# Kernel optimization log

Measured on AMD Instinct MI355X. Metric: run time of the kernel, lower is better.

## Reference

```python
import jax, jax.numpy as jnp
import numpy as np
from jax import lax

B, S, H, W = 16, 5, 64, 64
D, DS, DEPTH, EXPAND, NC = 128, 16, 2, 2, 2


def _ln(x, w, b, eps=1e-5):
    m = x.mean(-1, keepdims=True)
    v = ((x - m) ** 2).mean(-1, keepdims=True)
    return (x - m) / jnp.sqrt(v + eps) * w + b


def _conv2d(x, w, b, stride, pad):
    y = lax.conv_general_dilated(x, w, (stride, stride), [(pad, pad), (pad, pad)],
                                 dimension_numbers=('NCHW', 'OIHW', 'NCHW'))
    return y + b[None, :, None, None]


def _convT2d(x, w, b):
    # torch ConvTranspose2d(k=4, s=2, p=1); w: (Cin, Cout, 4, 4)
    k = jnp.transpose(w[:, :, ::-1, ::-1], (1, 0, 2, 3))
    y = lax.conv_general_dilated(x, k, (1, 1), [(2, 2), (2, 2)], lhs_dilation=(2, 2),
                                 dimension_numbers=('NCHW', 'OIHW', 'NCHW'))
    return y + b[None, :, None, None]


def _dwconv1d(x, w, b):
    # x: [B, L, D]; torch depthwise Conv1d k=4 pad=3 then truncate to L == left-pad 3
    y = lax.conv_general_dilated(x.transpose(0, 2, 1), w, (1,), [(3, 0)],
                                 feature_group_count=w.shape[0],
                                 dimension_numbers=('NCH', 'OIH', 'NCH'))
    return (y + b[None, :, None]).transpose(0, 2, 1)


def _selective_scan(x, ln_w, ln_b, in_w, in_b, x_w, x_b, A_log, Dm, out_w, out_b):
    xn = _ln(x, ln_w, ln_b)
    xz = xn @ in_w.T + in_b
    xp, z = jnp.split(xz, 2, axis=-1)
    xp = jax.nn.silu(xp)
    z = jax.nn.sigmoid(z)
    u = xp @ x_w.T + x_b                        # [B, L, DS]
    a = jnp.exp(-jnp.exp(A_log))[0, 0]          # [DS] decay factor exp(A), A = -exp(A_log)

    def step(h, u_t):
        h = a * h + u_t
        return h, h

    _, hs = lax.scan(step, jnp.zeros((x.shape[0], DS), x.dtype), u.transpose(1, 0, 2))
    hs = hs.transpose(1, 0, 2)                  # [B, L, DS]
    y = (hs @ Dm) * z
    y = y @ out_w.T + out_b                     # dropout is identity at inference
    return x + y


def setup_inputs() -> dict:
    key = jax.random.key(0)
    ks = iter(jax.random.split(key, 64))

    def nrm(shape, scale=0.02):
        return (jax.random.normal(next(ks), shape) * scale).astype(jnp.float32)

    d, ds, hw = D, DS, H * W
    return {
        'x': jax.random.normal(next(ks), (B, S, H, W), dtype=jnp.float32),
        'emb_w': nrm((d, 1, 3, 3), 0.1), 'emb_b': jnp.zeros((d,), jnp.float32),
        'pos_embed': nrm((hw, d)), 'time_embed': nrm((S, d)),
        'blk_ln1_w': jnp.ones((DEPTH, d), jnp.float32), 'blk_ln1_b': jnp.zeros((DEPTH, d), jnp.float32),
        'blk_conv_w': nrm((DEPTH, d, 1, 4), 0.2), 'blk_conv_b': jnp.zeros((DEPTH, d), jnp.float32),
        'blk_sln_w': jnp.ones((DEPTH, d), jnp.float32), 'blk_sln_b': jnp.zeros((DEPTH, d), jnp.float32),
        'blk_A_log': nrm((DEPTH, 1, 1, ds), 0.5),
        'blk_D': nrm((DEPTH, ds, d), 0.1),
        'blk_in_w': nrm((DEPTH, 2 * d, d), 0.05), 'blk_in_b': jnp.zeros((DEPTH, 2 * d), jnp.float32),
        'blk_x_w': nrm((DEPTH, ds, d), 0.05), 'blk_x_b': jnp.zeros((DEPTH, ds), jnp.float32),
        'blk_out_w': nrm((DEPTH, d, d), 0.05), 'blk_out_b': jnp.zeros((DEPTH, d), jnp.float32),
        'blk_ln2_w': jnp.ones((DEPTH, d), jnp.float32), 'blk_ln2_b': jnp.zeros((DEPTH, d), jnp.float32),
        'blk_mlp_w1': nrm((DEPTH, EXPAND * d, d), 0.05), 'blk_mlp_b1': jnp.zeros((DEPTH, EXPAND * d), jnp.float32),
        'blk_mlp_w2': nrm((DEPTH, d, EXPAND * d), 0.05), 'blk_mlp_b2': jnp.zeros((DEPTH, d), jnp.float32),
        'down1_w': nrm((d, d, 3, 3), 0.05), 'down1_b': jnp.zeros((d,), jnp.float32),
        'down2_w': nrm((2 * d, d, 3, 3), 0.05), 'down2_b': jnp.zeros((2 * d,), jnp.float32),
        'bott_w': nrm((2 * d, 2 * d, 3, 3), 0.05), 'bott_b': jnp.zeros((2 * d,), jnp.float32),
        'up1_w': nrm((2 * d, d, 4, 4), 0.05), 'up1_b': jnp.zeros((d,), jnp.float32),
        'up2_w': nrm((2 * d, d, 4, 4), 0.05), 'up2_b': jnp.zeros((d,), jnp.float32),
        'final_w': nrm((NC, 2 * d, 1, 1), 0.05), 'final_b': jnp.zeros((NC,), jnp.float32),
    }


def reference(x, emb_w, emb_b, pos_embed, time_embed,
              blk_ln1_w, blk_ln1_b, blk_conv_w, blk_conv_b,
              blk_sln_w, blk_sln_b, blk_A_log, blk_D,
              blk_in_w, blk_in_b, blk_x_w, blk_x_b, blk_out_w, blk_out_b,
              blk_ln2_w, blk_ln2_b, blk_mlp_w1, blk_mlp_b1, blk_mlp_w2, blk_mlp_b2,
              down1_w, down1_b, down2_w, down2_b, bott_w, bott_b,
              up1_w, up1_b, up2_w, up2_b, final_w, final_b):
    b, s, h, w = x.shape
    # embed all frames at once (linear combination weights: 0.5 each, last frame 1.0)
    e = _conv2d(x.reshape(b * s, 1, h, w), emb_w, emb_b, 1, 1)      # [B*S, D, H, W]
    e = e.reshape(b, s, D, h * w).transpose(0, 1, 3, 2)              # [B, S, HW, D]
    e = e + pos_embed[None, None] + time_embed[:s][None, :, None, :]
    wts = jnp.where(jnp.arange(s) == s - 1, 1.0, 0.5).astype(x.dtype)
    emb = jnp.einsum('bsld,s->bld', e, wts)                          # [B, HW, D]
    for i in range(DEPTH):
        xn = _ln(emb, blk_ln1_w[i], blk_ln1_b[i])
        emb = emb + _dwconv1d(xn, blk_conv_w[i], blk_conv_b[i])
        emb = _selective_scan(emb, blk_sln_w[i], blk_sln_b[i], blk_in_w[i], blk_in_b[i],
                              blk_x_w[i], blk_x_b[i], blk_A_log[i], blk_D[i],
                              blk_out_w[i], blk_out_b[i])
        m = _ln(emb, blk_ln2_w[i], blk_ln2_b[i])
        m = jax.nn.gelu(m @ blk_mlp_w1[i].T + blk_mlp_b1[i], approximate=False)
        emb = emb + (m @ blk_mlp_w2[i].T + blk_mlp_b2[i])
    sp = emb.transpose(0, 2, 1).reshape(b, D, h, w)
    x1 = jax.nn.relu(_conv2d(sp, down1_w, down1_b, 2, 1))
    x2 = jax.nn.relu(_conv2d(x1, down2_w, down2_b, 2, 1))
    x2 = jax.nn.relu(_conv2d(x2, bott_w, bott_b, 1, 1))
    u1 = jax.nn.relu(_convT2d(x2, up1_w, up1_b))
    u1 = jnp.concatenate([u1, x1], axis=1)
    u2 = jax.nn.relu(_convT2d(u1, up2_w, up2_b))
    u2 = jnp.concatenate([u2, sp], axis=1)
    return _conv2d(u2, final_w, final_b, 1, 0)
```

## Files before the change

### kernel.cpp

```cpp
#include <hip/hip_runtime.h>
#include <cmath>

namespace {
constexpr int Bn = 16, Ln = 4096, Dn = 128, DSn = 16;
constexpr int Mtok = Bn * Ln;
}

typedef short bfx8 __attribute__((ext_vector_type(8)));
typedef float f32x4 __attribute__((ext_vector_type(4)));

static __device__ __forceinline__ ushort f2bf(float f) {
  union { float f; unsigned u; } v; v.f = f;
  unsigned r = v.u + 0x7fff + ((v.u >> 16) & 1);
  return (ushort)(r >> 16);
}
static __device__ __forceinline__ float bf2f(ushort u) {
  union { unsigned u; float f; } v; v.u = ((unsigned)u) << 16;
  return v.f;
}

__global__ void k_prep(const float* __restrict__ inw, const float* __restrict__ outw,
                       const float* __restrict__ m1, const float* __restrict__ m2,
                       const float* __restrict__ xw, const float* __restrict__ cw,
                       const float* __restrict__ d1, const float* __restrict__ d2,
                       const float* __restrict__ bo, const float* __restrict__ u1,
                       const float* __restrict__ u2, ushort* __restrict__ W3,
                       float* __restrict__ CWT) {
  int i = blockIdx.x * 256 + threadIdx.x;
  if (i < 65536) { W3[i] = f2bf(inw[i]); return; }
  if (i < 98304) { W3[i] = f2bf(outw[i - 65536]); return; }
  if (i < 163840) { W3[i] = f2bf(m1[i - 98304]); return; }
  if (i < 229376) { W3[i] = f2bf(m2[i - 163840]); return; }
  if (i < 233472) { W3[i] = f2bf(xw[i - 229376]); return; }
  if (i < 234496) {
    int j = i - 233472; int blk = j >> 9, r = j & 511, d = r >> 2, k = r & 3;
    CWT[blk * 512 + k * 128 + d] = cw[j]; return;
  }
  if (i < 381952) {
    int j = i - 234496; int co = j / (128 * 9); int r = j - co * (128 * 9);
    int ci = r / 9, tap = r - ci * 9;
    W3[233472 + ((size_t)tap * 128 + co) * 128 + ci] = f2bf(d1[j]); return;
  }
  if (i < 676864) {
    int j = i - 381952; int co = j / (128 * 9); int r = j - co * (128 * 9);
    int ci = r / 9, tap = r - ci * 9;
    W3[380928 + ((size_t)tap * 256 + co) * 128 + ci] = f2bf(d2[j]); return;
  }
  if (i < 1266688) {
    int j = i - 676864; int co = j / (256 * 9); int r = j - co * (256 * 9);
    int ci = r / 9, tap = r - ci * 9;
    W3[675840 + ((size_t)tap * 256 + co) * 256 + ci] = f2bf(bo[j]); return;
  }
  if (i < 1790976) {
    int j = i - 1266688; int ci = j / (128 * 16); int r = j - ci * (128 * 16);
    int co = r >> 4, tap = r & 15;
    W3[1265664 + ((size_t)tap * 128 + co) * 256 + ci] = f2bf(u1[j]); return;
  }
  if (i < 2315264) {
    int j = i - 1790976; int ci = j / (128 * 16); int r = j - ci * (128 * 16);
    int co = r >> 4, tap = r & 15;
    W3[1789952 + ((size_t)tap * 128 + co) * 256 + ci] = f2bf(u2[j]); return;
  }
}

__global__ void k_combine(const float* __restrict__ x, float* __restrict__ xc) {
  int i = blockIdx.x * 256 + threadIdx.x;
  int b = i >> 12, p = i & 4095;
  const float* xb = x + (size_t)b * 5 * Ln + p;
  xc[i] = 0.5f * (xb[0] + xb[Ln] + xb[2 * Ln] + xb[3 * Ln]) + xb[4 * Ln];
}

__global__ __launch_bounds__(256) void k_embedln(
    const float* __restrict__ xc, const float* __restrict__ ew, const float* __restrict__ eb,
    const float* __restrict__ pos, const float* __restrict__ te,
    const float* __restrict__ lw, const float* __restrict__ lb,
    float* __restrict__ emb, ushort* __restrict__ xn) {
  int tok = blockIdx.x * 8 + (threadIdx.x >> 5);
  int ln = threadIdx.x & 31;
  int b = tok >> 12, l = tok & 4095;
  int h = l >> 6, w = l & 63;
  const float* xb = xc + b * 4096;
  float v[9];
#pragma unroll
  for (int dy = 0; dy < 3; dy++)
#pragma unroll
    for (int dx = 0; dx < 3; dx++) {
      int y = h + dy - 1, xx = w + dx - 1;
      v[dy * 3 + dx] = (y >= 0 && y < 64 && xx >= 0 && xx < 64) ? xb[y * 64 + xx] : 0.f;
    }
  int d0 = ln * 4;
  float o[4]; float s = 0.f, sq = 0.f;
#pragma unroll
  for (int e = 0; e < 4; e++) {
    int d = d0 + e;
    float a = 0.f;
#pragma unroll
    for (int k = 0; k < 9; k++) a += v[k] * ew[d * 9 + k];
    float ts = 0.5f * (te[d] + te[128 + d] + te[256 + d] + te[384 + d]) + te[512 + d];
    float r = a + 3.f * eb[d] + 3.f * pos[l * 128 + d] + ts;
    o[e] = r; s += r; sq += r * r;
  }
  float4 f4; f4.x = o[0]; f4.y = o[1]; f4.z = o[2]; f4.w = o[3];
  *(float4*)(emb + (size_t)tok * 128 + d0) = f4;
#pragma unroll
  for (int off = 16; off; off >>= 1) { s += __shfl_xor(s, off); sq += __shfl_xor(sq, off); }
  float m = s * (1.f / 128.f);
  float var = sq * (1.f / 128.f) - m * m;
  float rs = rsqrtf(var + 1e-5f);
  ushort4 u;
  u.x = f2bf((o[0] - m) * rs * lw[d0 + 0] + lb[d0 + 0]);
  u.y = f2bf((o[1] - m) * rs * lw[d0 + 1] + lb[d0 + 1]);
  u.z = f2bf((o[2] - m) * rs * lw[d0 + 2] + lb[d0 + 2]);
  u.w = f2bf((o[3] - m) * rs * lw[d0 + 3] + lb[d0 + 3]);
  *(ushort4*)(xn + (size_t)tok * 128 + d0) = u;
}

__global__ __launch_bounds__(256) void k_fuse1(
    const ushort* __restrict__ xn1, float* __restrict__ emb, ushort* __restrict__ xn2,
    const float* __restrict__ cwT, const float* __restrict__ cb,
    const float* __restrict__ sw, const float* __restrict__ sb) {
  int i = blockIdx.x * 256 + threadIdx.x;
  int g = i & 15, tok = i >> 4, d0 = g * 8, l = tok & 4095;
  const ushort* p = xn1 + (size_t)tok * 128 + d0;
  const bfx8 zf = {0, 0, 0, 0, 0, 0, 0, 0};
  bfx8 v0 = *(const bfx8*)p;
  bfx8 v1 = (l >= 1) ? *(const bfx8*)(p - 128) : zf;
  bfx8 v2 = (l >= 2) ? *(const bfx8*)(p - 256) : zf;
  bfx8 v3 = (l >= 3) ? *(const bfx8*)(p - 384) : zf;
  float* ep = emb + (size_t)tok * 128 + d0;
  float4 e0 = *(const float4*)ep;
  float4 e1 = *(const float4*)(ep + 4);
  float ev[8] = {e0.x, e0.y, e0.z, e0.w, e1.x, e1.y, e1.z, e1.w};
  float nv[8]; float s = 0.f, sq = 0.f;
#pragma unroll
  for (int e = 0; e < 8; e++) {
    int d = d0 + e;
    float c = cb[d] + cwT[3 * 128 + d] * bf2f((ushort)v0[e]) + cwT[2 * 128 + d] * bf2f((ushort)v1[e]) +
              cwT[1 * 128 + d] * bf2f((ushort)v2[e]) + cwT[0 * 128 + d] * bf2f((ushort)v3[e]);
    nv[e] = ev[e] + c;
    s += nv[e]; sq += nv[e] * nv[e];
  }
  float4 w0; w0.x = nv[0]; w0.y = nv[1]; w0.z = nv[2]; w0.w = nv[3];
  float4 w1; w1.x = nv[4]; w1.y = nv[5]; w1.z = nv[6]; w1.w = nv[7];
  *(float4*)ep = w0;
  *(float4*)(ep + 4) = w1;
#pragma unroll
  for (int off = 8; off; off >>= 1) { s += __shfl_xor(s, off); sq += __shfl_xor(sq, off); }
  float m = s * (1.f / 128.f);
  float var = sq * (1.f / 128.f) - m * m;
  float rs = rsqrtf(var + 1e-5f);
  bfx8 r8;
#pragma unroll
  for (int e = 0; e < 8; e++) {
    int d = d0 + e;
    r8[e] = (short)f2bf((nv[e] - m) * rs * sw[d] + sb[d]);
  }
  *(bfx8*)(xn2 + (size_t)tok * 128 + d0) = r8;
}

template <int MODE, int K>
__global__ __launch_bounds__(256) void k_mgemm(const ushort* __restrict__ A, const ushort* __restrict__ W,
                                               const float* __restrict__ bias, void* __restrict__ outv,
                                               void* __restrict__ out2v, float* __restrict__ emb,
                                               const float* __restrict__ lw, const float* __restrict__ lb) {
  __shared__ float red[2][128][2];
  const int t = threadIdx.x;
  const int l = t & 63, wv = t >> 6;
  const int l15 = l & 15, q = l >> 4;
  const int wm = wv >> 1, wn = wv & 1;
  const int m0 = blockIdx.x * 128 + wm * 64;
  const int n0 = blockIdx.y * 128 + wn * 64;
  f32x4 acc[4][4] = {};
  const ushort* Ab = A + (size_t)(m0 + l15) * K + q * 8;
  const ushort* Wb = W + (size_t)(n0 + l15) * K + q * 8;
#pragma unroll
  for (int k0 = 0; k0 < K; k0 += 32) {
    bfx8 a[4], b[4];
#pragma unroll
    for (int mf = 0; mf < 4; mf++) a[mf] = *(const bfx8*)(Ab + (size_t)mf * 16 * K + k0);
#pragma unroll
    for (int nf = 0; nf < 4; nf++) b[nf] = *(const bfx8*)(Wb + (size_t)nf * 16 * K + k0);
#pragma unroll
    for (int mf = 0; mf < 4; mf++)
#pragma unroll
      for (int nf = 0; nf < 4; nf++)
        acc[mf][nf] = __builtin_amdgcn_mfma_f32_16x16x32_bf16(a[mf], b[nf], acc[mf][nf], 0, 0, 0);
  }
  if constexpr (MODE == 1 || MODE == 2) {
#pragma unroll
    for (int mf = 0; mf < 4; mf++) {
#pragma unroll
      for (int nf = 0; nf < 4; nf++) {
        const int col = n0 + nf * 16 + l15;
        const float bb = bias[col];
#pragma unroll
        for (int r = 0; r < 4; r++) {
          const int row = m0 + mf * 16 + q * 4 + r;
          float v = acc[mf][nf][r] + bb;
          if (MODE == 1) {
            if (col < 128) {
              ((ushort*)outv)[(size_t)row * 128 + col] = f2bf(v / (1.f + expf(-v)));
            } else {
              ((ushort*)out2v)[(size_t)row * 128 + col - 128] = f2bf(1.f / (1.f + expf(-v)));
            }
          } else {
            ((ushort*)outv)[(size_t)row * 256 + col] = f2bf(0.5f * v * (1.f + erff(v * 0.7071067811865475f)));
          }
        }
      }
    }
  } else {
    float sv[4][4], qv[4][4];
#pragma unroll
    for (int mf = 0; mf < 4; mf++)
#pragma unroll
      for (int r = 0; r < 4; r++) { sv[mf][r] = 0.f; qv[mf][r] = 0.f; }
#pragma unroll
    for (int mf = 0; mf < 4; mf++) {
#pragma unroll
      for (int nf = 0; nf < 4; nf++) {
        const int col = n0 + nf * 16 + l15;
        const float bb = bias[col];
#pragma unroll
        for (int r = 0; r < 4; r++) {
          const int row = m0 + mf * 16 + q * 4 + r;
          float v = acc[mf][nf][r] + bb + emb[(size_t)row * 128 + col];
          acc[mf][nf][r] = v;
          sv[mf][r] += v; qv[mf][r] += v * v;
        }
      }
    }
    if constexpr (MODE == 5) {
#pragma unroll
      for (int mf = 0; mf < 4; mf++)
#pragma unroll
        for (int r = 0; r < 4; r++) {
#pragma unroll
          for (int off = 1; off < 16; off <<= 1) {
            sv[mf][r] += __shfl_xor(sv[mf][r], off);
            qv[mf][r] += __shfl_xor(qv[mf][r], off);
          }
          if (l15 == 0) {
            int rowl = wm * 64 + mf * 16 + q * 4 + r;
            red[0][rowl][wn] = sv[mf][r];
            red[1][rowl][wn] = qv[mf][r];
          }
        }
      __syncthreads();
    }
#pragma unroll
    for (int mf = 0; mf < 4; mf++)
#pragma unroll
      for (int r = 0; r < 4; r++) {
        const int rowl = wm * 64 + mf * 16 + q * 4 + r;
        const int row = blockIdx.x * 128 + rowl;
        float mm = 0.f, rs = 0.f;
        if constexpr (MODE == 5) {
          float ts = red[0][rowl][0] + red[0][rowl][1];
          float tq = red[1][rowl][0] + red[1][rowl][1];
          mm = ts * (1.f / 128.f);
          float var = tq * (1.f / 128.f) - mm * mm;
          rs = rsqrtf(var + 1e-5f);
        }
#pragma unroll
        for (int nf = 0; nf < 4; nf++) {
          const int col = n0 + nf * 16 + l15;
          float v = acc[mf][nf][r];
          emb[(size_t)row * 128 + col] = v;
          if constexpr (MODE == 5)
            ((ushort*)out2v)[(size_t)row * 128 + col] = f2bf((v - mm) * rs * lw[col] + lb[col]);
          else
            ((ushort*)out2v)[(size_t)row * 256 + 128 + col] = f2bf(v);
        }
      }
  }
}

__global__ __launch_bounds__(256) void k_ub(const ushort* __restrict__ XP, const ushort* __restrict__ xw,
                                            const float* __restrict__ xb, float* __restrict__ UT) {
  __shared__ float xs[16 * 132];
  __shared__ float wsm[16 * 129];
  const int m0 = blockIdx.x * 16;
  const int t = threadIdx.x;
  for (int idx = t; idx < 2048; idx += 256) {
    wsm[(idx >> 7) * 129 + (idx & 127)] = bf2f(xw[idx]);
    xs[(idx >> 7) * 132 + (idx & 127)] = bf2f(XP[(size_t)m0 * 128 + idx]);
  }
  __syncthreads();
  const int ds = t & 15, ml = t >> 4;
  float acc = 0.f;
#pragma unroll 16
  for (int k = 0; k < 128; k++) acc += xs[ml * 132 + k] * wsm[ds * 129 + k];
  const int b = m0 >> 12, l0 = m0 & 4095;
  UT[((size_t)(b * 16 + ds)) * 4096 + l0 + ml] = acc + xb[ds];
}

__global__ __launch_bounds__(64) void k_scan(const float* __restrict__ UT, float* __restrict__ HST,
                                             const float* __restrict__ A_log) {
  const int b = blockIdx.x >> 4, ds = blockIdx.x & 15;
  const int tid = threadIdx.x;
  const float a = expf(-expf(A_log[ds]));
  const float4* ut4 = (const float4*)(UT + ((size_t)(b * 16 + ds)) * 4096 + tid * 64);
  float r[64];
#pragma unroll
  for (int j4 = 0; j4 < 16; j4++) {
    float4 v = ut4[j4];
    r[j4 * 4 + 0] = v.x; r[j4 * 4 + 1] = v.y; r[j4 * 4 + 2] = v.z; r[j4 * 4 + 3] = v.w;
  }
  float h = 0.f;
#pragma unroll
  for (int j = 0; j < 64; j++) { h = a * h + r[j]; r[j] = h; }
  float a64 = a;
#pragma unroll
  for (int qq = 0; qq < 6; qq++) a64 *= a64;
  float Ac = a64, Bc = h;
#pragma unroll
  for (int off = 1; off < 64; off <<= 1) {
    float Ap = __shfl_up(Ac, off);
    float Bp = __shfl_up(Bc, off);
    if (tid >= off) { Bc = Ac * Bp + Bc; Ac = Ac * Ap; }
  }
  float carry = __shfl_up(Bc, 1);
  if (tid == 0) carry = 0.f;
  float p = a;
#pragma unroll
  for (int j = 0; j < 64; j++) { r[j] += p * carry; p *= a; }
  float4* hb4 = (float4*)(HST + ((size_t)(b * 16 + ds)) * 4096 + tid * 64);
#pragma unroll
  for (int j4 = 0; j4 < 16; j4++) {
    float4 v; v.x = r[j4 * 4 + 0]; v.y = r[j4 * 4 + 1]; v.z = r[j4 * 4 + 2]; v.w = r[j4 * 4 + 3];
    hb4[j4] = v;
  }
}

__global__ __launch_bounds__(256) void k_yb(const float* __restrict__ HST, const float* __restrict__ Dm_,
                                            const ushort* __restrict__ Z, ushort* __restrict__ Y) {
  const int m = blockIdx.x * 2 + (threadIdx.x >> 7);
  const int d = threadIdx.x & 127;
  const int b = m >> 12, l = m & 4095;
  const float* hb = HST + (size_t)b * 16 * Ln + l;
  float acc = 0.f;
#pragma unroll
  for (int s = 0; s < 16; s++) acc += hb[(size_t)s * Ln] * Dm_[s * 128 + d];
  const size_t o = (size_t)m * 128 + d;
  Y[o] = f2bf(acc * bf2f(Z[o]));
}

template <int MODE, int OTH, int OTW, int CIN>
__global__ __launch_bounds__(256) void k_cv(
    const ushort* __restrict__ in, ushort* __restrict__ out,
    const ushort* __restrict__ wt, const float* __restrict__ bias,
    int Hi, int Wi, int CP, int CO, int CPo, int COo, int Cout,
    int nsp, int nspx, long ibs, long obs) {
  constexpr int ITH = (MODE == 1) ? (2 * OTH + 1) : (OTH + 2);
  constexpr int ITW = (MODE == 1) ? (2 * OTW + 1) : (OTW + 2);
  constexpr int NPIX = ITH * ITW;
  constexpr int SPF = OTH * OTW / 16;
  constexpr int NTAPS = (MODE == 2) ? 4 : 9;
  constexpr int NCH = CIN / 32;
  __shared__ __attribute__((aligned(16))) ushort lds[NPIX * 40];
  const int t = threadIdx.x;
  const int w = t >> 6, l = t & 63;
  const int l15 = l & 15, q = l >> 4;
  const int b = blockIdx.z;
  const int py = (MODE == 2) ? ((int)blockIdx.y >> 1) : 0;
  const int px = (MODE == 2) ? ((int)blockIdx.y & 1) : 0;
  const int cb = blockIdx.x / nsp;
  const int spt = blockIdx.x - cb * nsp;
  const int spy = spt / nspx, spx = spt - spy * nspx;
  const int n0 = cb * 64 + w * 16;
  const int y0 = spy * OTH, x0 = spx * OTW;
  const int gy0 = (MODE == 1) ? (2 * y0 - 1) : (y0 - 1);
  const int gx0 = (MODE == 1) ? (2 * x0 - 1) : (x0 - 1);
  const ushort* ib = in + (size_t)b * ibs;
  f32x4 acc[SPF] = {};
  int abase[SPF];
#pragma unroll
  for (int af = 0; af < SPF; af++) {
    int p = af * 16 + l15;
    int ty = p / OTW, tx = p % OTW;
    int sy = (MODE == 1) ? (2 * ty) : ty;
    int sx = (MODE == 1) ? (2 * tx) : tx;
    abase[af] = (sy * ITW + sx) * 40 + q * 8;
  }
  for (int c = 0; c < NCH; c++) {
    const int k0 = c * 32;
    __syncthreads();
    for (int idx = t; idx < NPIX * 4; idx += 256) {
      int pix = idx >> 2, qq = idx & 3;
      int sy = pix / ITW, sx = pix - sy * ITW;
      int gy = gy0 + sy, gx = gx0 + sx;
      bfx8 v = {0, 0, 0, 0, 0, 0, 0, 0};
      if ((unsigned)gy < (unsigned)Hi && (unsigned)gx < (unsigned)Wi)
        v = *(const bfx8*)(ib + (size_t)(gy * Wi + gx) * CP + CO + k0 + qq * 8);
      *(bfx8*)&lds[pix * 40 + qq * 8] = v;
    }
    __syncthreads();
#pragma unroll
    for (int tap = 0; tap < NTAPS; tap++) {
      const int dy = (MODE == 2) ? (tap >> 1) : (tap / 3);
      const int dx = (MODE == 2) ? (tap & 1) : (tap - (tap / 3) * 3);
      const int tapw = (MODE == 2) ? ((3 - py - 2 * dy) * 4 + (3 - px - 2 * dx)) : tap;
      const int toff = (MODE == 2) ? (((py + dy) * ITW + (px + dx)) * 40)
                                   : ((dy * ITW + dx) * 40);
      bfx8 bv = *(const bfx8*)(wt + ((size_t)tapw * Cout + n0 + l15) * CIN + k0 + q * 8);
#pragma unroll
      for (int af = 0; af < SPF; af++) {
        bfx8 av = *(const bfx8*)&lds[abase[af] + toff];
        acc[af] = __builtin_amdgcn_mfma_f32_16x16x32_bf16(av, bv, acc[af], 0, 0, 0);
      }
    }
  }
  const float bb = bias[n0 + l15];
  ushort* ob = out + (size_t)b * obs + COo + n0 + l15;
#pragma unroll
  for (int af = 0; af < SPF; af++) {
#pragma unroll
    for (int r = 0; r < 4; r++) {
      int p = af * 16 + q * 4 + r;
      int ty = p / OTW, tx = p % OTW;
      int oy, ox, Wo;
      if (MODE == 2) { oy = (y0 + ty) * 2 + py; ox = (x0 + tx) * 2 + px; Wo = Wi * 2; }
      else if (MODE == 1) { oy = y0 + ty; ox = x0 + tx; Wo = Wi / 2; }
      else { oy = y0 + ty; ox = x0 + tx; Wo = Wi; }
      ob[(size_t)(oy * Wo + ox) * CPo] = f2bf(fmaxf(acc[af][r] + bb, 0.f));
    }
  }
}

__global__ void k_final2(const ushort* __restrict__ in, const float* __restrict__ w,
                         const float* __restrict__ bias, float* __restrict__ out) {
  int i = blockIdx.x * 256 + threadIdx.x;
  int b = i >> 12, p = i & 4095;
  const ushort* row = in + (size_t)i * 256;
  float a0 = bias[0], a1 = bias[1];
  for (int c = 0; c < 256; c += 4) {
    ushort4 u = *(const ushort4*)(row + c);
    float4 w0 = *(const float4*)(w + c);
    float4 w1 = *(const float4*)(w + 256 + c);
    float f0 = bf2f(u.x), f1 = bf2f(u.y), f2 = bf2f(u.z), f3 = bf2f(u.w);
    a0 += f0 * w0.x + f1 * w0.y + f2 * w0.z + f3 * w0.w;
    a1 += f0 * w1.x + f1 * w1.y + f2 * w1.z + f3 * w1.w;
  }
  out[(size_t)b * 8192 + p] = a0;
  out[(size_t)b * 8192 + 4096 + p] = a1;
}

extern "C" void kernel_launch(void* const* d_in, const int* in_sizes, int n_in,
                              void* d_out, int out_size, void* d_ws, size_t ws_size,
                              hipStream_t stream) {
  (void)in_sizes; (void)n_in; (void)out_size; (void)ws_size;
  const float* x          = (const float*)d_in[0];
  const float* emb_w      = (const float*)d_in[1];
  const float* emb_b      = (const float*)d_in[2];
  const float* pos_embed  = (const float*)d_in[3];
  const float* time_embed = (const float*)d_in[4];
  const float* blk_ln1_w  = (const float*)d_in[5];
  const float* blk_ln1_b  = (const float*)d_in[6];
  const float* blk_conv_w = (const float*)d_in[7];
  const float* blk_conv_b = (const float*)d_in[8];
  const float* blk_sln_w  = (const float*)d_in[9];
  const float* blk_sln_b  = (const float*)d_in[10];
  const float* blk_A_log  = (const float*)d_in[11];
  const float* blk_D      = (const float*)d_in[12];
  const float* blk_in_w   = (const float*)d_in[13];
  const float* blk_in_b   = (const float*)d_in[14];
  const float* blk_x_w    = (const float*)d_in[15];
  const float* blk_x_b    = (const float*)d_in[16];
  const float* blk_out_w  = (const float*)d_in[17];
  const float* blk_out_b  = (const float*)d_in[18];
  const float* blk_ln2_w  = (const float*)d_in[19];
  const float* blk_ln2_b  = (const float*)d_in[20];
  const float* blk_mlp_w1 = (const float*)d_in[21];
  const float* blk_mlp_b1 = (const float*)d_in[22];
  const float* blk_mlp_w2 = (const float*)d_in[23];
  const float* blk_mlp_b2 = (const float*)d_in[24];
  const float* down1_w    = (const float*)d_in[25];
  const float* down1_b    = (const float*)d_in[26];
  const float* down2_w    = (const float*)d_in[27];
  const float* down2_b    = (const float*)d_in[28];
  const float* bott_w     = (const float*)d_in[29];
  const float* bott_b     = (const float*)d_in[30];
  const float* up1_w      = (const float*)d_in[31];
  const float* up1_b      = (const float*)d_in[32];
  const float* up2_w      = (const float*)d_in[33];
  const float* up2_b      = (const float*)d_in[34];
  const float* final_w    = (const float*)d_in[35];
  const float* final_b    = (const float*)d_in[36];

  float* ws = (float*)d_ws;
  constexpr size_t F = 1u << 20;
  float* EMB = ws;
  ushort* XN1 = (ushort*)(ws + 8 * F);
  ushort* XN2 = XN1 + 8 * F;
  ushort* XPu = (ushort*)(ws + 16 * F);
  ushort* Zu  = XPu + 8 * F;
  ushort* MH  = XPu;
  ushort* W3  = (ushort*)(ws + 24 * F);
  float* Ubuf = ws + 32 * F;
  float* HST  = ws + 33 * F;

  ushort* Wi  = W3;
  ushort* Wo  = W3 + 65536;
  ushort* Wm1 = W3 + 98304;
  ushort* Wm2 = W3 + 163840;
  ushort* Wx  = W3 + 229376;
  ushort* Wd1 = W3 + 233472;
  ushort* Wd2 = W3 + 380928;
  ushort* Wb9 = W3 + 675840;
  ushort* Wu1 = W3 + 1265664;
  ushort* Wu2 = W3 + 1789952;
  float*  CWT = (float*)(W3 + 2314240);

  k_prep<<<9044, 256, 0, stream>>>(blk_in_w, blk_out_w, blk_mlp_w1, blk_mlp_w2, blk_x_w,
                                   blk_conv_w, down1_w, down2_w, bott_w, up1_w, up2_w, W3, CWT);
  k_combine<<<256, 256, 0, stream>>>(x, Ubuf);
  k_embedln<<<8192, 256, 0, stream>>>(Ubuf, emb_w, emb_b, pos_embed, time_embed,
                                      blk_ln1_w, blk_ln1_b, EMB, XN1);

  ushort* U2C = XPu;
  for (int i = 0; i < 2; i++) {
    k_fuse1<<<4096, 256, 0, stream>>>(XN1, EMB, XN2, CWT + i * 512, blk_conv_b + i * Dn,
                                      blk_sln_w + i * Dn, blk_sln_b + i * Dn);
    k_mgemm<1, 128><<<dim3(512, 2), 256, 0, stream>>>(XN2, Wi + i * 32768, blk_in_b + i * 256,
                                                      XPu, Zu, nullptr, nullptr, nullptr);
    k_ub<<<4096, 256, 0, stream>>>(XPu, Wx + i * 2048, blk_x_b + i * DSn, Ubuf);
    k_scan<<<256, 64, 0, stream>>>(Ubuf, HST, blk_A_log + i * DSn);
    k_yb<<<32768, 256, 0, stream>>>(HST, blk_D + i * DSn * Dn, Zu, XN2);
    k_mgemm<5, 128><<<dim3(512, 1), 256, 0, stream>>>(XN2, Wo + i * 16384, blk_out_b + i * Dn,
                                                      nullptr, XN1, EMB,
                                                      blk_ln2_w + i * Dn, blk_ln2_b + i * Dn);
    k_mgemm<2, 128><<<dim3(512, 2), 256, 0, stream>>>(XN1, Wm1 + i * 32768, blk_mlp_b1 + i * 256,
                                                      MH, nullptr, nullptr, nullptr, nullptr);
    if (i == 0)
      k_mgemm<5, 256><<<dim3(512, 1), 256, 0, stream>>>(MH, Wm2 + i * 32768, blk_mlp_b2 + i * Dn,
                                                        nullptr, XN1, EMB,
                                                        blk_ln1_w + Dn, blk_ln1_b + Dn);
    else
      k_mgemm<4, 256><<<dim3(512, 1), 256, 0, stream>>>(MH, Wm2 + i * 32768, blk_mlp_b2 + i * Dn,
                                                        nullptr, U2C, EMB, nullptr, nullptr);
  }

  ushort* U1C = XN1;
  ushort* X2b = XN1 + 8388608;
  ushort* X3b = X2b + 1048576;

  k_cv<1, 8, 8, 128><<<dim3(2 * 16, 1, 16), 256, 0, stream>>>(
      U2C, U1C, Wd1, down1_b, 64, 64, 256, 128, 256, 128, 128,
      16, 4, 64L * 64 * 256, 32L * 32 * 256);
  k_cv<1, 8, 8, 128><<<dim3(4 * 4, 1, 16), 256, 0, stream>>>(
      U1C, X2b, Wd2, down2_b, 32, 32, 256, 128, 256, 0, 256,
      4, 2, 32L * 32 * 256, 16L * 16 * 256);
  k_cv<0, 8, 8, 256><<<dim3(4 * 4, 1, 16), 256, 0, stream>>>(
      X2b, X3b, Wb9, bott_b, 16, 16, 256, 0, 256, 0, 256,
      4, 2, 16L * 16 * 256, 16L * 16 * 256);
  k_cv<2, 8, 16, 256><<<dim3(2 * 2, 4, 16), 256, 0, stream>>>(
      X3b, U1C, Wu1, up1_b, 16, 16, 256, 0, 256, 0, 128,
      2, 1, 16L * 16 * 256, 32L * 32 * 256);
  k_cv<2, 16, 16, 256><<<dim3(2 * 4, 4, 16), 256, 0, stream>>>(
      U1C, U2C, Wu2, up2_b, 32, 32, 256, 0, 256, 0, 128,
      4, 2, 32L * 32 * 256, 64L * 64 * 256);

  k_final2<<<256, 256, 0, stream>>>(U2C, final_w, final_b, (float*)d_out);
}
```

Baseline: 554.5 us.

## Fuse in-proj with x-proj GEMM and out-proj with MLP-up GEMM via LDS

The input-projection GEMM now keeps the SiLU branch tile in shared memory and computes the 16-wide x-projection with MFMA in the same kernel. This removes the separate k_ub kernel and the XP round trip through global memory. The output projection plus LayerNorm is likewise fused with the first MLP GEMM plus GELU, keeping the normalized tile in LDS so XN1 is no longer written and reread. The conv kernels gain a waves-per-block template parameter, and the smaller decoder layers now launch more blocks of 128 threads. The cost is extra LDS and register pressure in the fused kernels, and a serial second GEMM per block.

```diff
diff --git a/kernel.cpp b/kernel.cpp
--- a/kernel.cpp
+++ b/kernel.cpp
@@ -4,6 +4,7 @@
 namespace {
 constexpr int Bn = 16, Ln = 4096, Dn = 128, DSn = 16;
 constexpr int Mtok = Bn * Ln;
+constexpr int SLS = 138;
 }
 
 typedef short bfx8 __attribute__((ext_vector_type(8)));
@@ -158,10 +159,206 @@
   *(bfx8*)(xn2 + (size_t)tok * 128 + d0) = r8;
 }
 
+__global__ __launch_bounds__(256) void k_gemm_xz(
+    const ushort* __restrict__ A, const ushort* __restrict__ W, const float* __restrict__ bias,
+    ushort* __restrict__ Zu, const ushort* __restrict__ xw, const float* __restrict__ xb,
+    float* __restrict__ UT) {
+  __shared__ ushort sl[128 * SLS];
+  const int t = threadIdx.x;
+  const int l = t & 63, wv = t >> 6;
+  const int l15 = l & 15, q = l >> 4;
+  const int wm = wv >> 1, wn = wv & 1;
+  const int m0 = blockIdx.x * 128 + wm * 64;
+  const int n0 = blockIdx.y * 128 + wn * 64;
+  f32x4 acc[4][4] = {};
+  const ushort* Ab = A + (size_t)(m0 + l15) * 128 + q * 8;
+  const ushort* Wb = W + (size_t)(n0 + l15) * 128 + q * 8;
+#pragma unroll
+  for (int k0 = 0; k0 < 128; k0 += 32) {
+    bfx8 a[4], b[4];
+#pragma unroll
+    for (int mf = 0; mf < 4; mf++) a[mf] = *(const bfx8*)(Ab + (size_t)mf * 16 * 128 + k0);
+#pragma unroll
+    for (int nf = 0; nf < 4; nf++) b[nf] = *(const bfx8*)(Wb + (size_t)nf * 16 * 128 + k0);
+#pragma unroll
+    for (int mf = 0; mf < 4; mf++)
+#pragma unroll
+      for (int nf = 0; nf < 4; nf++)
+        acc[mf][nf] = __builtin_amdgcn_mfma_f32_16x16x32_bf16(a[mf], b[nf], acc[mf][nf], 0, 0, 0);
+  }
+  if (blockIdx.y == 1) {
+#pragma unroll
+    for (int mf = 0; mf < 4; mf++)
+#pragma unroll
+      for (int nf = 0; nf < 4; nf++) {
+        const int col = n0 + nf * 16 + l15;
+        const float bb = bias[col];
+#pragma unroll
+        for (int r = 0; r < 4; r++) {
+          const int row = m0 + mf * 16 + q * 4 + r;
+          float v = acc[mf][nf][r] + bb;
+          Zu[(size_t)row * 128 + col - 128] = f2bf(1.f / (1.f + expf(-v)));
+        }
+      }
+    return;
+  }
+#pragma unroll
+  for (int mf = 0; mf < 4; mf++)
+#pragma unroll
+    for (int nf = 0; nf < 4; nf++) {
+      const int col = wn * 64 + nf * 16 + l15;
+      const float bb = bias[col];
+#pragma unroll
+      for (int r = 0; r < 4; r++) {
+        const int rowl = wm * 64 + mf * 16 + q * 4 + r;
+        float v = acc[mf][nf][r] + bb;
+        sl[rowl * SLS + col] = f2bf(v / (1.f + expf(-v)));
+      }
+    }
+  __syncthreads();
+  f32x4 pu[2] = {};
+#pragma unroll
+  for (int k0 = 0; k0 < 128; k0 += 32) {
+    bfx8 bx_ = *(const bfx8*)(xw + l15 * 128 + k0 + q * 8);
+#pragma unroll
+    for (int mi = 0; mi < 2; mi++) {
+      bfx8 a2 = *(const bfx8*)&sl[(wv * 32 + mi * 16 + l15) * SLS + k0 + q * 8];
+      pu[mi] = __builtin_amdgcn_mfma_f32_16x16x32_bf16(a2, bx_, pu[mi], 0, 0, 0);
+    }
+  }
+  const float ub = xb[l15];
+#pragma unroll
+  for (int mi = 0; mi < 2; mi++)
+#pragma unroll
+    for (int r = 0; r < 4; r++) {
+      int token = blockIdx.x * 128 + wv * 32 + mi * 16 + q * 4 + r;
+      int b = token >> 12, ll = token & 4095;
+      UT[((size_t)(b * 16 + l15)) * 4096 + ll] = pu[mi][r] + ub;
+    }
+}
+
+__global__ __launch_bounds__(256) void k_gemm_om(
+    const ushort* __restrict__ A, const ushort* __restrict__ W1, const float* __restrict__ b1,
+    float* __restrict__ emb, const float* __restrict__ lw, const float* __restrict__ lb,
+    const ushort* __restrict__ W2, const float* __restrict__ b2, ushort* __restrict__ MH) {
+  __shared__ ushort sl[128 * SLS];
+  __shared__ float red[2][128][2];
+  const int t = threadIdx.x;
+  const int l = t & 63, wv = t >> 6;
+  const int l15 = l & 15, q = l >> 4;
+  const int wm = wv >> 1, wn = wv & 1;
+  const int m0 = blockIdx.x * 128 + wm * 64;
+  const int n0 = wn * 64;
+  {
+    f32x4 acc[4][4] = {};
+    const ushort* Ab = A + (size_t)(m0 + l15) * 128 + q * 8;
+    const ushort* Wb = W1 + (size_t)(n0 + l15) * 128 + q * 8;
+#pragma unroll
+    for (int k0 = 0; k0 < 128; k0 += 32) {
+      bfx8 a[4], b[4];
+#pragma unroll
+      for (int mf = 0; mf < 4; mf++) a[mf] = *(const bfx8*)(Ab + (size_t)mf * 16 * 128 + k0);
+#pragma unroll
+      for (int nf = 0; nf < 4; nf++) b[nf] = *(const bfx8*)(Wb + (size_t)nf * 16 * 128 + k0);
+#pragma unroll
+      for (int mf = 0; mf < 4; mf++)
+#pragma unroll
+        for (int nf = 0; nf < 4; nf++)
+          acc[mf][nf] = __builtin_amdgcn_mfma_f32_16x16x32_bf16(a[mf], b[nf], acc[mf][nf], 0, 0, 0);
+    }
+    float sv[4][4], qv[4][4];
+#pragma unroll
+    for (int mf = 0; mf < 4; mf++)
+#pragma unroll
+      for (int r = 0; r < 4; r++) { sv[mf][r] = 0.f; qv[mf][r] = 0.f; }
+#pragma unroll
+    for (int mf = 0; mf < 4; mf++)
+#pragma unroll
+      for (int nf = 0; nf < 4; nf++) {
+        const int col = n0 + nf * 16 + l15;
+        const float bb = b1[col];
+#pragma unroll
+        for (int r = 0; r < 4; r++) {
+          const int row = m0 + mf * 16 + q * 4 + r;
+          float v = acc[mf][nf][r] + bb + emb[(size_t)row * 128 + col];
+          acc[mf][nf][r] = v;
+          sv[mf][r] += v; qv[mf][r] += v * v;
+        }
+      }
+#pragma unroll
+    for (int mf = 0; mf < 4; mf++)
+#pragma unroll
+      for (int r = 0; r < 4; r++) {
+#pragma unroll
+        for (int off = 1; off < 16; off <<= 1) {
+          sv[mf][r] += __shfl_xor(sv[mf][r], off);
+          qv[mf][r] += __shfl_xor(qv[mf][r], off);
+        }
+        if (l15 == 0) {
+          int rowl = wm * 64 + mf * 16 + q * 4 + r;
+          red[0][rowl][wn] = sv[mf][r];
+          red[1][rowl][wn] = qv[mf][r];
+        }
+      }
+    __syncthreads();
+#pragma unroll
+    for (int mf = 0; mf < 4; mf++)
+#pragma unroll
+      for (int r = 0; r < 4; r++) {
+        const int rowl = wm * 64 + mf * 16 + q * 4 + r;
+        const int row = blockIdx.x * 128 + rowl;
+        float ts = red[0][rowl][0] + red[0][rowl][1];
+        float tq = red[1][rowl][0] + red[1][rowl][1];
+        float mm = ts * (1.f / 128.f);
+        float var = tq * (1.f / 128.f) - mm * mm;
+        float rs = rsqrtf(var + 1e-5f);
+#pragma unroll
+        for (int nf = 0; nf < 4; nf++) {
+          const int col = n0 + nf * 16 + l15;
+          float v = acc[mf][nf][r];
+          emb[(size_t)row * 128 + col] = v;
+          sl[rowl * SLS + col] = f2bf((v - mm) * rs * lw[col] + lb[col]);
+        }
+      }
+  }
+  __syncthreads();
+#pragma unroll
+  for (int p = 0; p < 2; p++) {
+    f32x4 acc2[2][8] = {};
+#pragma unroll
+    for (int k0 = 0; k0 < 128; k0 += 32) {
+      bfx8 a2[2];
+#pragma unroll
+      for (int mi = 0; mi < 2; mi++)
+        a2[mi] = *(const bfx8*)&sl[(wv * 32 + mi * 16 + l15) * SLS + k0 + q * 8];
+#pragma unroll
+      for (int nf = 0; nf < 8; nf++) {
+        bfx8 b2v = *(const bfx8*)(W2 + (size_t)(p * 128 + nf * 16 + l15) * 128 + k0 + q * 8);
+#pragma unroll
+        for (int mi = 0; mi < 2; mi++)
+          acc2[mi][nf] = __builtin_amdgcn_mfma_f32_16x16x32_bf16(a2[mi], b2v, acc2[mi][nf], 0, 0, 0);
+      }
+    }
+#pragma unroll
+    for (int mi = 0; mi < 2; mi++)
+#pragma unroll
+      for (int nf = 0; nf < 8; nf++) {
+        const int col = p * 128 + nf * 16 + l15;
+        const float bb = b2[col];
+#pragma unroll
+        for (int r = 0; r < 4; r++) {
+          const int row = blockIdx.x * 128 + wv * 32 + mi * 16 + q * 4 + r;
+          float v = acc2[mi][nf][r] + bb;
+          MH[(size_t)row * 256 + col] = f2bf(0.5f * v * (1.f + erff(v * 0.7071067811865475f)));
+        }
+      }
+  }
+}
+
 template <int MODE, int K>
 __global__ __launch_bounds__(256) void k_mgemm(const ushort* __restrict__ A, const ushort* __restrict__ W,
-                                               const float* __restrict__ bias, void* __restrict__ outv,
-                                               void* __restrict__ out2v, float* __restrict__ emb,
+                                               const float* __restrict__ bias, void* __restrict__ out2v,
+                                               float* __restrict__ emb,
                                                const float* __restrict__ lw, const float* __restrict__ lb) {
   __shared__ float red[2][128][2];
   const int t = threadIdx.x;
@@ -169,7 +366,7 @@
   const int l15 = l & 15, q = l >> 4;
   const int wm = wv >> 1, wn = wv & 1;
   const int m0 = blockIdx.x * 128 + wm * 64;
-  const int n0 = blockIdx.y * 128 + wn * 64;
+  const int n0 = wn * 64;
   f32x4 acc[4][4] = {};
   const ushort* Ab = A + (size_t)(m0 + l15) * K + q * 8;
   const ushort* Wb = W + (size_t)(n0 + l15) * K + q * 8;
@@ -186,113 +383,68 @@
       for (int nf = 0; nf < 4; nf++)
         acc[mf][nf] = __builtin_amdgcn_mfma_f32_16x16x32_bf16(a[mf], b[nf], acc[mf][nf], 0, 0, 0);
   }
-  if constexpr (MODE == 1 || MODE == 2) {
-#pragma unroll
-    for (int mf = 0; mf < 4; mf++) {
+  float sv[4][4], qv[4][4];
+#pragma unroll
+  for (int mf = 0; mf < 4; mf++)
+#pragma unroll
+    for (int r = 0; r < 4; r++) { sv[mf][r] = 0.f; qv[mf][r] = 0.f; }
+#pragma unroll
+  for (int mf = 0; mf < 4; mf++)
+#pragma unroll
+    for (int nf = 0; nf < 4; nf++) {
+      const int col = n0 + nf * 16 + l15;
+      const float bb = bias[col];
+#pragma unroll
+      for (int r = 0; r < 4; r++) {
+        const int row = m0 + mf * 16 + q * 4 + r;
+        float v = acc[mf][nf][r] + bb + emb[(size_t)row * 128 + col];
+        acc[mf][nf][r] = v;
+        sv[mf][r] += v; qv[mf][r] += v * v;
+      }
+    }
+  if constexpr (MODE == 5) {
+#pragma unroll
+    for (int mf = 0; mf < 4; mf++)
+#pragma unroll
+      for (int r = 0; r < 4; r++) {
+#pragma unroll
+        for (int off = 1; off < 16; off <<= 1) {
+          sv[mf][r] += __shfl_xor(sv[mf][r], off);
+          qv[mf][r] += __shfl_xor(qv[mf][r], off);
+        }
+        if (l15 == 0) {
+          int rowl = wm * 64 + mf * 16 + q * 4 + r;
+          red[0][rowl][wn] = sv[mf][r];
+          red[1][rowl][wn] = qv[mf][r];
+        }
+      }
+    __syncthreads();
+  }
+#pragma unroll
+  for (int mf = 0; mf < 4; mf++)
+#pragma unroll
+    for (int r = 0; r < 4; r++) {
+      const int rowl = wm * 64 + mf * 16 + q * 4 + r;
+      const int row = blockIdx.x * 128 + rowl;
+      float mm = 0.f, rs = 0.f;
+      if constexpr (MODE == 5) {
+        float ts = red[0][rowl][0] + red[0][rowl][1];
+        float tq = red[1][rowl][0] + red[1][rowl][1];
+        mm = ts * (1.f / 128.f);
+        float var = tq * (1.f / 128.f) - mm * mm;
+        rs = rsqrtf(var + 1e-5f);
+      }
 #pragma unroll
       for (int nf = 0; nf < 4; nf++) {
         const int col = n0 + nf * 16 + l15;
-        const float bb = bias[col];
-#pragma unroll
-        for (int r = 0; r < 4; r++) {
-          const int row = m0 + mf * 16 + q * 4 + r;
-          float v = acc[mf][nf][r] + bb;
-          if (MODE == 1) {
-            if (col < 128) {
-              ((ushort*)outv)[(size_t)row * 128 + col] = f2bf(v / (1.f + expf(-v)));
-            } else {
-              ((ushort*)out2v)[(size_t)row * 128 + col - 128] = f2bf(1.f / (1.f + expf(-v)));
-            }
-          } else {
-            ((ushort*)outv)[(size_t)row * 256 + col] = f2bf(0.5f * v * (1.f + erff(v * 0.7071067811865475f)));
-          }
-        }
-      }
-    }
-  } else {
-    float sv[4][4], qv[4][4];
-#pragma unroll
-    for (int mf = 0; mf < 4; mf++)
-#pragma unroll
-      for (int r = 0; r < 4; r++) { sv[mf][r] = 0.f; qv[mf][r] = 0.f; }
-#pragma unroll
-    for (int mf = 0; mf < 4; mf++) {
-#pragma unroll
-      for (int nf = 0; nf < 4; nf++) {
-        const int col = n0 + nf * 16 + l15;
-        const float bb = bias[col];
-#pragma unroll
-        for (int r = 0; r < 4; r++) {
-          const int row = m0 + mf * 16 + q * 4 + r;
-          float v = acc[mf][nf][r] + bb + emb[(size_t)row * 128 + col];
-          acc[mf][nf][r] = v;
-          sv[mf][r] += v; qv[mf][r] += v * v;
-        }
-      }
-    }
-    if constexpr (MODE == 5) {
-#pragma unroll
-      for (int mf = 0; mf < 4; mf++)
-#pragma unroll
-        for (int r = 0; r < 4; r++) {
-#pragma unroll
-          for (int off = 1; off < 16; off <<= 1) {
-            sv[mf][r] += __shfl_xor(sv[mf][r], off);
-            qv[mf][r] += __shfl_xor(qv[mf][r], off);
-          }
-          if (l15 == 0) {
-            int rowl = wm * 64 + mf * 16 + q * 4 + r;
-            red[0][rowl][wn] = sv[mf][r];
-            red[1][rowl][wn] = qv[mf][r];
-          }
-        }
-      __syncthreads();
-    }
-#pragma unroll
-    for (int mf = 0; mf < 4; mf++)
-#pragma unroll
-      for (int r = 0; r < 4; r++) {
-        const int rowl = wm * 64 + mf * 16 + q * 4 + r;
-        const int row = blockIdx.x * 128 + rowl;
-        float mm = 0.f, rs = 0.f;
-        if constexpr (MODE == 5) {
-          float ts = red[0][rowl][0] + red[0][rowl][1];
-          float tq = red[1][rowl][0] + red[1][rowl][1];
-          mm = ts * (1.f / 128.f);
-          float var = tq * (1.f / 128.f) - mm * mm;
-          rs = rsqrtf(var + 1e-5f);
-        }
-#pragma unroll
-        for (int nf = 0; nf < 4; nf++) {
-          const int col = n0 + nf * 16 + l15;
-          float v = acc[mf][nf][r];
-          emb[(size_t)row * 128 + col] = v;
-          if constexpr (MODE == 5)
-            ((ushort*)out2v)[(size_t)row * 128 + col] = f2bf((v - mm) * rs * lw[col] + lb[col]);
-          else
-            ((ushort*)out2v)[(size_t)row * 256 + 128 + col] = f2bf(v);
-        }
-      }
-  }
-}
-
-__global__ __launch_bounds__(256) void k_ub(const ushort* __restrict__ XP, const ushort* __restrict__ xw,
-                                            const float* __restrict__ xb, float* __restrict__ UT) {
-  __shared__ float xs[16 * 132];
-  __shared__ float wsm[16 * 129];
-  const int m0 = blockIdx.x * 16;
-  const int t = threadIdx.x;
-  for (int idx = t; idx < 2048; idx += 256) {
-    wsm[(idx >> 7) * 129 + (idx & 127)] = bf2f(xw[idx]);
-    xs[(idx >> 7) * 132 + (idx & 127)] = bf2f(XP[(size_t)m0 * 128 + idx]);
-  }
-  __syncthreads();
-  const int ds = t & 15, ml = t >> 4;
-  float acc = 0.f;
-#pragma unroll 16
-  for (int k = 0; k < 128; k++) acc += xs[ml * 132 + k] * wsm[ds * 129 + k];
-  const int b = m0 >> 12, l0 = m0 & 4095;
-  UT[((size_t)(b * 16 + ds)) * 4096 + l0 + ml] = acc + xb[ds];
+        float v = acc[mf][nf][r];
+        emb[(size_t)row * 128 + col] = v;
+        if constexpr (MODE == 5)
+          ((ushort*)out2v)[(size_t)row * 128 + col] = f2bf((v - mm) * rs * lw[col] + lb[col]);
+        else
+          ((ushort*)out2v)[(size_t)row * 256 + 128 + col] = f2bf(v);
+      }
+    }
 }
 
 __global__ __launch_bounds__(64) void k_scan(const float* __restrict__ UT, float* __restrict__ HST,
@@ -346,8 +498,8 @@
   Y[o] = f2bf(acc * bf2f(Z[o]));
 }
 
-template <int MODE, int OTH, int OTW, int CIN>
-__global__ __launch_bounds__(256) void k_cv(
+template <int MODE, int OTH, int OTW, int CIN, int WPB>
+__global__ __launch_bounds__(WPB * 64) void k_cv(
     const ushort* __restrict__ in, ushort* __restrict__ out,
     const ushort* __restrict__ wt, const float* __restrict__ bias,
     int Hi, int Wi, int CP, int CO, int CPo, int COo, int Cout,
@@ -368,7 +520,7 @@
   const int cb = blockIdx.x / nsp;
   const int spt = blockIdx.x - cb * nsp;
   const int spy = spt / nspx, spx = spt - spy * nspx;
-  const int n0 = cb * 64 + w * 16;
+  const int n0 = cb * (16 * WPB) + w * 16;
   const int y0 = spy * OTH, x0 = spx * OTW;
   const int gy0 = (MODE == 1) ? (2 * y0 - 1) : (y0 - 1);
   const int gx0 = (MODE == 1) ? (2 * x0 - 1) : (x0 - 1);
@@ -386,7 +538,7 @@
   for (int c = 0; c < NCH; c++) {
     const int k0 = c * 32;
     __syncthreads();
-    for (int idx = t; idx < NPIX * 4; idx += 256) {
+    for (int idx = t; idx < NPIX * 4; idx += WPB * 64) {
       int pix = idx >> 2, qq = idx & 3;
       int sy = pix / ITW, sx = pix - sy * ITW;
       int gy = gy0 + sy, gx = gx0 + sx;
@@ -493,10 +645,9 @@
   float* EMB = ws;
   ushort* XN1 = (ushort*)(ws + 8 * F);
   ushort* XN2 = XN1 + 8 * F;
-  ushort* XPu = (ushort*)(ws + 16 * F);
-  ushort* Zu  = XPu + 8 * F;
-  ushort* MH  = XPu;
-  ushort* W3  = (ushort*)(ws + 24 * F);
+  ushort* MH  = (ushort*)(ws + 16 * F);
+  ushort* Zu  = (ushort*)(ws + 24 * F);
+  ushort* W3  = (ushort*)(ws + 28 * F);
   float* Ubuf = ws + 32 * F;
   float* HST  = ws + 33 * F;
 
@@ -518,46 +669,42 @@
   k_embedln<<<8192, 256, 0, stream>>>(Ubuf, emb_w, emb_b, pos_embed, time_embed,
                                       blk_ln1_w, blk_ln1_b, EMB, XN1);
 
-  ushort* U2C = XPu;
+  ushort* U2C = MH;
   for (int i = 0; i < 2; i++) {
     k_fuse1<<<4096, 256, 0, stream>>>(XN1, EMB, XN2, CWT + i * 512, blk_conv_b + i * Dn,
                                       blk_sln_w + i * Dn, blk_sln_b + i * Dn);
-    k_mgemm<1, 128><<<dim3(512, 2), 256, 0, stream>>>(XN2, Wi + i * 32768, blk_in_b + i * 256,
-                                                      XPu, Zu, nullptr, nullptr, nullptr);
-    k_ub<<<4096, 256, 0, stream>>>(XPu, Wx + i * 2048, blk_x_b + i * DSn, Ubuf);
+    k_gemm_xz<<<dim3(512, 2), 256, 0, stream>>>(XN2, Wi + i * 32768, blk_in_b + i * 256,
+                                                Zu, Wx + i * 2048, blk_x_b + i * DSn, Ubuf);
     k_scan<<<256, 64, 0, stream>>>(Ubuf, HST, blk_A_log + i * DSn);
     k_yb<<<32768, 256, 0, stream>>>(HST, blk_D + i * DSn * Dn, Zu, XN2);
-    k_mgemm<5, 128><<<dim3(512, 1), 256, 0, stream>>>(XN2, Wo + i * 16384, blk_out_b + i * Dn,
-                                                      nullptr, XN1, EMB,
-                                                      blk_ln2_w + i * Dn, blk_ln2_b + i * Dn);
-    k_mgemm<2, 128><<<dim3(512, 2), 256, 0, stream>>>(XN1, Wm1 + i * 32768, blk_mlp_b1 + i * 256,
-                                                      MH, nullptr, nullptr, nullptr, nullptr);
+    k_gemm_om<<<dim3(512, 1), 256, 0, stream>>>(XN2, Wo + i * 16384, blk_out_b + i * Dn,
+                                                EMB, blk_ln2_w + i * Dn, blk_ln2_b + i * Dn,
+                                                Wm1 + i * 32768, blk_mlp_b1 + i * 256, MH);
     if (i == 0)
       k_mgemm<5, 256><<<dim3(512, 1), 256, 0, stream>>>(MH, Wm2 + i * 32768, blk_mlp_b2 + i * Dn,
-                                                        nullptr, XN1, EMB,
-                                                        blk_ln1_w + Dn, blk_ln1_b + Dn);
+                                                        XN1, EMB, blk_ln1_w + Dn, blk_ln1_b + Dn);
     else
       k_mgemm<4, 256><<<dim3(512, 1), 256, 0, stream>>>(MH, Wm2 + i * 32768, blk_mlp_b2 + i * Dn,
-                                                        nullptr, U2C, EMB, nullptr, nullptr);
+                                                        U2C, EMB, nullptr, nullptr);
   }
 
   ushort* U1C = XN1;
   ushort* X2b = XN1 + 8388608;
   ushort* X3b = X2b + 1048576;
 
-  k_cv<1, 8, 8, 128><<<dim3(2 * 16, 1, 16), 256, 0, stream>>>(
+  k_cv<1, 8, 8, 128, 4><<<dim3(2 * 16, 1, 16), 256, 0, stream>>>(
       U2C, U1C, Wd1, down1_b, 64, 64, 256, 128, 256, 128, 128,
       16, 4, 64L * 64 * 256, 32L * 32 * 256);
-  k_cv<1, 8, 8, 128><<<dim3(4 * 4, 1, 16), 256, 0, stream>>>(
+  k_cv<1, 8, 8, 128, 2><<<dim3(8 * 4, 1, 16), 128, 0, stream>>>(
       U1C, X2b, Wd2, down2_b, 32, 32, 256, 128, 256, 0, 256,
       4, 2, 32L * 32 * 256, 16L * 16 * 256);
-  k_cv<0, 8, 8, 256><<<dim3(4 * 4, 1, 16), 256, 0, stream>>>(
+  k_cv<0, 8, 8, 256, 2><<<dim3(8 * 4, 1, 16), 128, 0, stream>>>(
       X2b, X3b, Wb9, bott_b, 16, 16, 256, 0, 256, 0, 256,
       4, 2, 16L * 16 * 256, 16L * 16 * 256);
-  k_cv<2, 8, 16, 256><<<dim3(2 * 2, 4, 16), 256, 0, stream>>>(
+  k_cv<2, 8, 16, 256, 2><<<dim3(4 * 2, 4, 16), 128, 0, stream>>>(
       X3b, U1C, Wu1, up1_b, 16, 16, 256, 0, 256, 0, 128,
       2, 1, 16L * 16 * 256, 32L * 32 * 256);
-  k_cv<2, 16, 16, 256><<<dim3(2 * 4, 4, 16), 256, 0, stream>>>(
+  k_cv<2, 16, 16, 256, 4><<<dim3(2 * 4, 4, 16), 256, 0, stream>>>(
       U1C, U2C, Wu2, up2_b, 32, 32, 256, 0, 256, 0, 128,
       4, 2, 32L * 32 * 256, 64L * 64 * 256);
 
```

Measured after the change: 503.5 us. 1.1x faster.
